# Kernel optimization log

Hardware: AMD Instinct MI355X
Metric: run time of the kernel (lower is better)

Reference implementation:

```python
import jax, jax.numpy as jnp
import numpy as np

N, E, D, H, HD, DFF = 2048, 32768, 256, 8, 32, 1024
NEG = -1e30  # masked-out logit (exp -> 0 in fp32)


def _layer_norm(x, w, b, eps=1e-5):
    mu = jnp.mean(x, axis=-1, keepdims=True)
    var = jnp.mean((x - mu) ** 2, axis=-1, keepdims=True)
    return (x - mu) * jax.lax.rsqrt(var + eps) * w + b


def setup_inputs() -> dict:
    key = jax.random.key(0)
    ks = jax.random.split(key, 24)
    w = lambda k, shape: (jax.random.normal(k, shape, dtype=jnp.float32) * 0.02)
    inp = {
        "node_feat": jax.random.normal(ks[0], (N, D), dtype=jnp.float32),
        "edge_feat": jax.random.normal(ks[1], (E, 10), dtype=jnp.float32),
        "src": jax.random.randint(ks[2], (E,), 0, N),
        "dst": jax.random.randint(ks[3], (E,), 0, N),
        "Wq": w(ks[4], (D, D)), "bq": jnp.zeros((D,), jnp.float32),
        "Wk": w(ks[5], (D, D)), "bk": jnp.zeros((D,), jnp.float32),
        "Wv": w(ks[6], (D, D)), "bv": jnp.zeros((D,), jnp.float32),
        "Wo": w(ks[7], (D, D)), "bo": jnp.zeros((D,), jnp.float32),
        "We": w(ks[8], (10, H)), "be": jnp.zeros((H,), jnp.float32),
        "n1w": jnp.ones((D,), jnp.float32), "n1b": jnp.zeros((D,), jnp.float32),
        "W1": w(ks[9], (D, DFF)), "b1": jnp.zeros((DFF,), jnp.float32),
        "W2": w(ks[10], (DFF, D)), "b2": jnp.zeros((D,), jnp.float32),
        "n2w": jnp.ones((D,), jnp.float32), "n2b": jnp.zeros((D,), jnp.float32),
    }
    return inp


def reference(node_feat, edge_feat, src, dst, Wq, bq, Wk, bk, Wv, bv, Wo, bo,
              We, be, n1w, n1b, W1, b1, W2, b2, n2w, n2b):
    n = node_feat.shape[0]
    Q = (node_feat @ Wq + bq).reshape(n, H, HD)
    K = (node_feat @ Wk + bk).reshape(n, H, HD)
    V = (node_feat @ Wv + bv).reshape(n, H, HD)

    # dense [n, n, H] scores (faithful to the original dense blowup)
    scores = jnp.einsum('ihd,jhd->ijh', Q, K) / np.sqrt(HD).astype(np.float32)

    # scatter edge bias into dense matrix (last-write semantics like torch indexing)
    edge_bias = edge_feat @ We + be                       # [E, H]
    bias = jnp.zeros((n, n, H), jnp.float32).at[src, dst].set(edge_bias)
    scores = scores + bias

    # symmetric adjacency mask with self-loops
    adj = jnp.zeros((n, n), jnp.float32)
    adj = adj.at[src, dst].set(1.0).at[dst, src].set(1.0)
    idx = jnp.arange(n)
    adj = adj.at[idx, idx].set(1.0)

    scores = jnp.where(adj[:, :, None] > 0, scores, NEG)
    attn = jax.nn.softmax(scores, axis=1)                 # softmax over j (dim=1)

    out = jnp.einsum('ijh,jhd->ihd', attn, V).reshape(n, D)
    out = out @ Wo + bo
    out = _layer_norm(out + node_feat, n1w, n1b)
    ffn = jax.nn.relu(out @ W1 + b1) @ W2 + b2
    out = _layer_norm(out + ffn, n2w, n2b)
    return out
```

## Files before the change

### kernel.cpp

```cpp
#include <hip/hip_runtime.h>
#include <hip/hip_bf16.h>

#define NN 2048
#define E_CNT 32768
#define D 256
#define DFF 1024
#define MAXN 256

typedef __hip_bfloat16 bf16;
typedef __attribute__((ext_vector_type(8))) short short8;
typedef __attribute__((ext_vector_type(4))) float f32x4;

__device__ __forceinline__ short bf2s(bf16 x) { union { bf16 b; short s; } u; u.b = x; return u.s; }
__device__ __forceinline__ float bs2f(unsigned short v) { return __uint_as_float(((unsigned)v) << 16); }

__device__ __forceinline__ int sniff_flag(const unsigned short* p, int* sh)
{
    int tid = threadIdx.x;
    int cnt = 0;
    for (int t = tid; t < 512; t += 256) {
        float f = bs2f(p[t]);
        if (!(fabsf(f) < 1000.f)) cnt++;
    }
#pragma unroll
    for (int off = 32; off > 0; off >>= 1) cnt += __shfl_down(cnt, off, 64);
    if ((tid & 63) == 0) sh[tid >> 6] = cnt;
    __syncthreads();
    int tot = sh[0] + sh[1] + sh[2] + sh[3];
    return tot > 16;
}

struct PrepArgs {
    const void* node; const void* edge;
    const int* src; const int* dst;
    const void* We; const void* be;
    const void* wsrc[6];
    const void* ssrc[10]; int sn[10]; int soff[10];
    bf16* node_b16; float* node_f32; float* smalls;
    short* wt; float* eb; int* pair; unsigned* bits;
    int* flagp;
};

__global__ __launch_bounds__(256) void k_prep(PrepArgs A)
{
    __shared__ int sh[4];
    __shared__ short tile[32][33];
    __shared__ float wsm[80], bbs[8];
    const int b = blockIdx.x;
    const int t = threadIdx.x;

    if (b >= 1408 && b < 1536) {
        int e = (b - 1408) * 256 + t;
        if (e < E_CNT) {
            int s = A.src[e], d = A.dst[e];
            atomicMax(&A.pair[(size_t)s * NN + d], e);
            atomicOr(&A.bits[s * 64 + (d >> 5)], 1u << (d & 31));
            atomicOr(&A.bits[d * 64 + (s >> 5)], 1u << (s & 31));
        }
        int n = (b - 1408) * 16 + (t >> 4);
        if (t < 128 && n < NN) atomicOr(&A.bits[n * 64 + (n >> 5)], 1u << (n & 31));
        return;
    }

    const int flag = sniff_flag((const unsigned short*)A.node, sh);

    if (b < 768) {
        int a, ti, ntn;
        if (b < 256)      { a = b >> 6; ti = b & 63;  ntn = 8;  }
        else if (b < 512) { a = 4;      ti = b - 256; ntn = 32; }
        else              { a = 5;      ti = b - 512; ntn = 8;  }
        const int Kd = (a == 5) ? 1024 : 256;
        const int Nd = (a == 4) ? 1024 : 256;
        int n0 = (ti % ntn) * 32, k0 = (ti / ntn) * 32;
        const void* s = A.wsrc[a];
        int c = t & 31, r4 = t >> 5;
#pragma unroll
        for (int p = 0; p < 4; p++) {
            int r = r4 + p * 8;
            short v;
            if (flag) v = bf2s(__float2bfloat16(((const float*)s)[(size_t)(k0 + r) * Nd + n0 + c]));
            else      v = ((const short*)s)[(size_t)(k0 + r) * Nd + n0 + c];
            tile[r][c] = v;
        }
        __syncthreads();
        static const int woff[6] = {0, 65536, 131072, 196608, 262144, 524288};
        short* dT = A.wt + woff[a];
#pragma unroll
        for (int p = 0; p < 4; p++) {
            int r = r4 + p * 8;
            dT[(size_t)(n0 + r) * Kd + k0 + c] = tile[c][r];
        }
        return;
    }
    if (b < 1024) {
        int i0 = (b - 768) * 2048 + t;
        if (flag) {
            const float* s = (const float*)A.node;
#pragma unroll
            for (int k = 0; k < 8; k++) A.node_b16[i0 + k * 256] = __float2bfloat16(s[i0 + k * 256]);
        } else {
            const short* s = (const short*)A.node;
            short* d = (short*)A.node_b16;
#pragma unroll
            for (int k = 0; k < 8; k++) d[i0 + k * 256] = s[i0 + k * 256];
        }
        return;
    }
    if (b < 1280) {
        int i0 = (b - 1024) * 2048 + t;
        if (flag) {
            const float* s = (const float*)A.node;
#pragma unroll
            for (int k = 0; k < 8; k++) A.node_f32[i0 + k * 256] = s[i0 + k * 256];
        } else {
            const bf16* s = (const bf16*)A.node;
#pragma unroll
            for (int k = 0; k < 8; k++) A.node_f32[i0 + k * 256] = __bfloat162float(s[i0 + k * 256]);
        }
        return;
    }
    if (b < 1408) {
        if (t < 80) wsm[t] = flag ? ((const float*)A.We)[t] : __bfloat162float(((const bf16*)A.We)[t]);
        if (t < 8)  bbs[t] = flag ? ((const float*)A.be)[t] : __bfloat162float(((const bf16*)A.be)[t]);
        __syncthreads();
        int e = (b - 1280) * 256 + t;
        float v[10];
        if (flag) {
            const float* ef = (const float*)A.edge;
#pragma unroll
            for (int k = 0; k < 10; k++) v[k] = ef[e * 10 + k];
        } else {
            const bf16* ef = (const bf16*)A.edge;
#pragma unroll
            for (int k = 0; k < 10; k++) v[k] = __bfloat162float(ef[e * 10 + k]);
        }
#pragma unroll
        for (int h = 0; h < 8; h++) {
            float s = bbs[h];
#pragma unroll
            for (int k = 0; k < 10; k++) s += v[k] * wsm[k * 8 + h];
            A.eb[e * 8 + h] = s;
        }
        return;
    }
    if (t == 0) *A.flagp = flag;
    for (int a = 0; a < 10; a++) {
        int n = A.sn[a];
        float* d = A.smalls + A.soff[a];
        if (flag) {
            const float* s = (const float*)A.ssrc[a];
            for (int i = t; i < n; i += 256) d[i] = s[i];
        } else {
            const bf16* s = (const bf16*)A.ssrc[a];
            for (int i = t; i < n; i += 256) d[i] = __bfloat162float(s[i]);
        }
    }
}

__global__ __launch_bounds__(256) void k_qkv3(
    const bf16* __restrict__ A,
    const bf16* __restrict__ WqT, const bf16* __restrict__ WkT, const bf16* __restrict__ WvT,
    const float* __restrict__ bq, const float* __restrict__ bk, const float* __restrict__ bv,
    bf16* __restrict__ Qb, bf16* __restrict__ Kb, bf16* __restrict__ Vb)
{
    int z = blockIdx.z;
    const bf16* BT = (z == 0) ? WqT : (z == 1) ? WkT : WvT;
    const float* bias = (z == 0) ? bq : (z == 1) ? bk : bv;
    bf16* C = (z == 0) ? Qb : (z == 1) ? Kb : Vb;
    __shared__ __align__(16) short As[2][4 * 64 * 8];
    __shared__ __align__(16) short Bs[2][4 * 32 * 8];
    int t = threadIdx.x, w = t >> 6, l = t & 63, fr = l & 15, fc = l >> 4;
    int i0 = blockIdx.x * 64, j0 = blockIdx.y * 32;
    int lr = t >> 2, lc = t & 3;
    f32x4 acc0 = {0.f, 0.f, 0.f, 0.f}, acc1 = {0.f, 0.f, 0.f, 0.f};
    const short* ap = (const short*)A + (size_t)(i0 + lr) * D + lc * 8;
    const short* bp = (const short*)BT + (size_t)(j0 + (lr & 31)) * D + lc * 8;
    for (int k0 = 0; k0 < D; k0 += 64) {
        short8 av0 = *(const short8*)(ap + k0);
        short8 av1 = *(const short8*)(ap + k0 + 32);
        short8 bv0 = {}, bv1 = {};
        if (t < 128) {
            bv0 = *(const short8*)(bp + k0);
            bv1 = *(const short8*)(bp + k0 + 32);
        }
        __syncthreads();
        *(short8*)&As[0][(lc * 64 + lr) * 8] = av0;
        *(short8*)&As[1][(lc * 64 + lr) * 8] = av1;
        if (t < 128) {
            *(short8*)&Bs[0][(lc * 32 + lr) * 8] = bv0;
            *(short8*)&Bs[1][(lc * 32 + lr) * 8] = bv1;
        }
        __syncthreads();
#pragma unroll
        for (int s = 0; s < 2; s++) {
            short8 af  = *(const short8*)&As[s][(fc * 64 + w * 16 + fr) * 8];
            short8 bf0 = *(const short8*)&Bs[s][(fc * 32 + fr) * 8];
            short8 bf1 = *(const short8*)&Bs[s][(fc * 32 + 16 + fr) * 8];
            acc0 = __builtin_amdgcn_mfma_f32_16x16x32_bf16(af, bf0, acc0, 0, 0, 0);
            acc1 = __builtin_amdgcn_mfma_f32_16x16x32_bf16(af, bf1, acc1, 0, 0, 0);
        }
    }
    float bb0 = bias[j0 + fr], bb1 = bias[j0 + 16 + fr];
    int orow = i0 + w * 16 + fc * 4;
#pragma unroll
    for (int j = 0; j < 4; j++) {
        C[(size_t)(orow + j) * D + j0 + fr]      = __float2bfloat16(acc0[j] + bb0);
        C[(size_t)(orow + j) * D + j0 + 16 + fr] = __float2bfloat16(acc1[j] + bb1);
    }
}

template<int EPI>
__global__ __launch_bounds__(256) void k_gemm(
    const bf16* __restrict__ A, const bf16* __restrict__ BT,
    const float* __restrict__ bias, void* __restrict__ Cp, int N, int K)
{
    __shared__ __align__(16) short As[2][4 * 64 * 8];
    __shared__ __align__(16) short Bs[2][4 * 32 * 8];
    int t = threadIdx.x;
    int w = t >> 6, l = t & 63;
    int fr = l & 15, fc = l >> 4;
    int i0 = blockIdx.x * 64, j0 = blockIdx.y * 32;
    int lr = t >> 2, lc = t & 3;
    f32x4 acc0 = {0.f, 0.f, 0.f, 0.f}, acc1 = {0.f, 0.f, 0.f, 0.f};
    const short* ap = (const short*)A + (size_t)(i0 + lr) * K + lc * 8;
    const short* bp = (const short*)BT + (size_t)(j0 + (lr & 31)) * K + lc * 8;
    for (int k0 = 0; k0 < K; k0 += 64) {
        short8 av0 = *(const short8*)(ap + k0);
        short8 av1 = *(const short8*)(ap + k0 + 32);
        short8 bv0 = {}, bv1 = {};
        if (t < 128) {
            bv0 = *(const short8*)(bp + k0);
            bv1 = *(const short8*)(bp + k0 + 32);
        }
        __syncthreads();
        *(short8*)&As[0][(lc * 64 + lr) * 8] = av0;
        *(short8*)&As[1][(lc * 64 + lr) * 8] = av1;
        if (t < 128) {
            *(short8*)&Bs[0][(lc * 32 + lr) * 8] = bv0;
            *(short8*)&Bs[1][(lc * 32 + lr) * 8] = bv1;
        }
        __syncthreads();
#pragma unroll
        for (int s = 0; s < 2; s++) {
            short8 af  = *(const short8*)&As[s][(fc * 64 + w * 16 + fr) * 8];
            short8 bf0 = *(const short8*)&Bs[s][(fc * 32 + fr) * 8];
            short8 bf1 = *(const short8*)&Bs[s][(fc * 32 + 16 + fr) * 8];
            acc0 = __builtin_amdgcn_mfma_f32_16x16x32_bf16(af, bf0, acc0, 0, 0, 0);
            acc1 = __builtin_amdgcn_mfma_f32_16x16x32_bf16(af, bf1, acc1, 0, 0, 0);
        }
    }
    float bb0 = bias[j0 + fr];
    float bb1 = bias[j0 + 16 + fr];
    int orow = i0 + w * 16 + fc * 4;
    bf16* C = (bf16*)Cp;
#pragma unroll
    for (int j = 0; j < 4; j++) {
        C[(size_t)(orow + j) * N + j0 + fr]      = __float2bfloat16(fmaxf(acc0[j] + bb0, 0.f));
        C[(size_t)(orow + j) * N + j0 + 16 + fr] = __float2bfloat16(fmaxf(acc1[j] + bb1, 0.f));
    }
}

__global__ __launch_bounds__(256) void k_attn(
    const bf16* __restrict__ Q, const bf16* __restrict__ K,
    const bf16* __restrict__ V, const float* __restrict__ eb,
    const int* __restrict__ pair, const unsigned* __restrict__ bits,
    bf16* __restrict__ attn_out)
{
    int i = blockIdx.x;
    int tid = threadIdx.x;
    __shared__ float q[D];
    __shared__ int   nbr[MAXN];
    __shared__ int   eid[MAXN];
    __shared__ float sc[MAXN][8];
    __shared__ float lhi[8];
    __shared__ int   nn_s;
    q[tid] = bs2f(((const unsigned short*)Q)[(size_t)i * D + tid]);
    if (tid < 64) {
        unsigned wrd = bits[i * 64 + tid];
        int cnt = __popc(wrd);
        int pre = cnt;
#pragma unroll
        for (int off = 1; off < 64; off <<= 1) {
            int v = __shfl_up(pre, off, 64);
            if (tid >= off) pre += v;
        }
        int pos = pre - cnt;
        while (wrd) {
            int b = __ffs(wrd) - 1;
            wrd &= wrd - 1;
            if (pos < MAXN) nbr[pos] = tid * 32 + b;
            pos++;
        }
        if (tid == 63) nn_s = (pre < MAXN) ? pre : MAXN;
    }
    __syncthreads();
    int nn = nn_s;
    const size_t prow = (size_t)i * NN;
    for (int n = tid; n < nn; n += 256) eid[n] = pair[prow + nbr[n]];
    __syncthreads();
    const short* Ks = (const short*)K;
    for (int t2 = tid; t2 < nn * 8; t2 += 256) {
        int n = t2 >> 3, h = t2 & 7;
        int j = nbr[n];
        const short8* kr = (const short8*)(Ks + (size_t)j * D + h * 32);
        const float4* qr = (const float4*)(q + h * 32);
        float s = 0.f;
#pragma unroll
        for (int c = 0; c < 4; c++) {
            short8 kv = kr[c];
            float4 q0 = qr[c * 2], q1 = qr[c * 2 + 1];
            s += q0.x * bs2f((unsigned short)kv[0]) + q0.y * bs2f((unsigned short)kv[1])
               + q0.z * bs2f((unsigned short)kv[2]) + q0.w * bs2f((unsigned short)kv[3])
               + q1.x * bs2f((unsigned short)kv[4]) + q1.y * bs2f((unsigned short)kv[5])
               + q1.z * bs2f((unsigned short)kv[6]) + q1.w * bs2f((unsigned short)kv[7]);
        }
        s *= 0.17677669529663687f;
        int e = eid[n];
        if (e >= 0) s += eb[e * 8 + h];
        sc[n][h] = s;
    }
    __syncthreads();
    {
        int h = tid >> 5, l32 = tid & 31;
        float m = -1e30f;
        for (int n = l32; n < nn; n += 32) m = fmaxf(m, sc[n][h]);
#pragma unroll
        for (int off = 1; off < 32; off <<= 1) m = fmaxf(m, __shfl_xor(m, off, 64));
        float lsum = 0.f;
        for (int n = l32; n < nn; n += 32) {
            float e = __expf(sc[n][h] - m);
            sc[n][h] = e;
            lsum += e;
        }
#pragma unroll
        for (int off = 1; off < 32; off <<= 1) lsum += __shfl_xor(lsum, off, 64);
        if (l32 == 0) lhi[h] = 1.f / lsum;
    }
    __syncthreads();
    int h = tid >> 5;
    const unsigned short* Vu = (const unsigned short*)V;
    float acc = 0.f;
    int n = 0;
    for (; n + 4 <= nn; n += 4) {
        int j0 = nbr[n], j1 = nbr[n + 1], j2 = nbr[n + 2], j3 = nbr[n + 3];
        float p0 = sc[n][h], p1 = sc[n + 1][h], p2 = sc[n + 2][h], p3 = sc[n + 3][h];
        acc += p0 * bs2f(Vu[(size_t)j0 * D + tid]) + p1 * bs2f(Vu[(size_t)j1 * D + tid])
             + p2 * bs2f(Vu[(size_t)j2 * D + tid]) + p3 * bs2f(Vu[(size_t)j3 * D + tid]);
    }
    for (; n < nn; n++) acc += sc[n][h] * bs2f(Vu[(size_t)nbr[n] * D + tid]);
    attn_out[(size_t)i * D + tid] = __float2bfloat16(acc * lhi[h]);
}

template<int MODE, int KDIM>
__global__ __launch_bounds__(256) void k_gemmln(
    const bf16* __restrict__ A, const bf16* __restrict__ BT,
    const float* __restrict__ bias, const float* __restrict__ res,
    const float* __restrict__ lnw, const float* __restrict__ lnb,
    float* __restrict__ outf, bf16* __restrict__ outb, const int* __restrict__ flagp)
{
    __shared__ __align__(16) short As[4 * 32 * 8];
    __shared__ __align__(16) short Bs[4 * 256 * 8];
    __shared__ float Cs[32][257];
    int t = threadIdx.x;
    int w = t >> 6, l = t & 63, fr = l & 15, fc = l >> 4;
    int i0 = blockIdx.x * 32;
    int ar = t >> 2, akc = t & 3;
    f32x4 acc[2][4];
#pragma unroll
    for (int rt = 0; rt < 2; rt++)
#pragma unroll
        for (int c = 0; c < 4; c++) acc[rt][c] = {0.f, 0.f, 0.f, 0.f};
    const short* ap = (const short*)A + (size_t)(i0 + (ar & 31)) * KDIM + akc * 8;
    const short* bp = (const short*)BT;
    short8 av = {};
    if (t < 128) av = *(const short8*)(ap);
    short8 bv[4];
#pragma unroll
    for (int p = 0; p < 4; p++)
        bv[p] = *(const short8*)(bp + (size_t)(p * 64 + ar) * KDIM + akc * 8);
    for (int k0 = 0; k0 < KDIM; k0 += 32) {
        __syncthreads();
        if (t < 128) *(short8*)&As[(akc * 32 + ar) * 8] = av;
#pragma unroll
        for (int p = 0; p < 4; p++)
            *(short8*)&Bs[(akc * 256 + p * 64 + ar) * 8] = bv[p];
        __syncthreads();
        if (k0 + 32 < KDIM) {
            if (t < 128) av = *(const short8*)(ap + k0 + 32);
#pragma unroll
            for (int p = 0; p < 4; p++)
                bv[p] = *(const short8*)(bp + (size_t)(p * 64 + ar) * KDIM + k0 + 32 + akc * 8);
        }
        short8 af0 = *(const short8*)&As[(fc * 32 + fr) * 8];
        short8 af1 = *(const short8*)&As[(fc * 32 + 16 + fr) * 8];
#pragma unroll
        for (int c = 0; c < 4; c++) {
            int ct = w * 4 + c;
            short8 bfr = *(const short8*)&Bs[(fc * 256 + ct * 16 + fr) * 8];
            acc[0][c] = __builtin_amdgcn_mfma_f32_16x16x32_bf16(af0, bfr, acc[0][c], 0, 0, 0);
            acc[1][c] = __builtin_amdgcn_mfma_f32_16x16x32_bf16(af1, bfr, acc[1][c], 0, 0, 0);
        }
    }
#pragma unroll
    for (int rt = 0; rt < 2; rt++)
#pragma unroll
        for (int c = 0; c < 4; c++) {
            int ct = w * 4 + c;
            float bb = bias[ct * 16 + fr];
#pragma unroll
            for (int j = 0; j < 4; j++)
                Cs[rt * 16 + fc * 4 + j][ct * 16 + fr] = acc[rt][c][j] + bb;
        }
    __syncthreads();
    int r = t >> 3, c0 = t & 7;
    float vbuf[32];
    float s = 0.f, qq = 0.f;
#pragma unroll
    for (int m = 0; m < 32; m++) {
        int c = c0 + m * 8;
        float v = Cs[r][c] + res[(size_t)(i0 + r) * D + c];
        vbuf[m] = v;
        s += v; qq += v * v;
    }
#pragma unroll
    for (int off = 1; off < 8; off <<= 1) {
        s  += __shfl_xor(s, off, 64);
        qq += __shfl_xor(qq, off, 64);
    }
    float mu  = s * (1.f / D);
    float var = qq * (1.f / D) - mu * mu;
    float rsd = rsqrtf(var + 1e-5f);
    int flag = (MODE == 1) ? *flagp : 0;
#pragma unroll
    for (int m = 0; m < 32; m++) {
        int c = c0 + m * 8;
        float o = (vbuf[m] - mu) * rsd * lnw[c] + lnb[c];
        size_t idx = (size_t)(i0 + r) * D + c;
        if (MODE == 0) {
            outf[idx] = o;
            outb[idx] = __float2bfloat16(o);
        } else {
            if (flag) outf[idx] = o;
            else      outb[idx] = __float2bfloat16(o);
        }
    }
}

extern "C" void kernel_launch(void* const* d_in, const int* in_sizes, int n_in,
                              void* d_out, int out_size, void* d_ws, size_t ws_size,
                              hipStream_t stream)
{
    (void)in_sizes; (void)n_in; (void)out_size; (void)ws_size;

    char* ws = (char*)d_ws;
    const size_t KB = 1024;
    float*    conv     = (float*)ws;
    bf16*     node_b16 = (bf16*)(ws + 3584 * KB);
    short*    wt       = (short*)(ws + 4608 * KB);
    int*      flagp    = (int*)(ws + 6144 * KB);
    unsigned* bits     = (unsigned*)(ws + 6272 * KB);
    float*    eb       = (float*)(ws + 7168 * KB);
    bf16*     Qb       = (bf16*)(ws + 8192 * KB);
    bf16*     Kb       = (bf16*)(ws + 10240 * KB);
    bf16*     Vb       = (bf16*)(ws + 11264 * KB);
    bf16*     attn_out = (bf16*)(ws + 12288 * KB);
    float*    x1f      = (float*)(ws + 13312 * KB);
    bf16*     x1b      = (bf16*)(ws + 15360 * KB);
    int*      pair     = (int*)(ws + 16384 * KB);
    bf16*     hid      = (bf16*)(ws + 34816 * KB);

    float* node_f32 = conv;
    float* smalls   = conv + 524288;
    static const int sidx[10] = {5, 7, 9, 11, 14, 15, 17, 19, 20, 21};
    static const int ssz[10]  = {256, 256, 256, 256, 256, 256, 1024, 256, 256, 256};
    int soff[10]; int so = 0;
    for (int a = 0; a < 10; a++) { soff[a] = so; so += ssz[a]; }
    const float* fbq  = smalls + soff[0];
    const float* fbk  = smalls + soff[1];
    const float* fbv  = smalls + soff[2];
    const float* fbo  = smalls + soff[3];
    const float* fn1w = smalls + soff[4];
    const float* fn1b = smalls + soff[5];
    const float* fb1  = smalls + soff[6];
    const float* fb2  = smalls + soff[7];
    const float* fn2w = smalls + soff[8];
    const float* fn2b = smalls + soff[9];

    static const int widx[6] = {4, 6, 8, 10, 16, 18};
    const bf16* WqT = (const bf16*)(wt + 0);
    const bf16* WkT = (const bf16*)(wt + 65536);
    const bf16* WvT = (const bf16*)(wt + 131072);
    const bf16* WoT = (const bf16*)(wt + 196608);
    const bf16* W1T = (const bf16*)(wt + 262144);
    const bf16* W2T = (const bf16*)(wt + 524288);

    PrepArgs pa;
    pa.node = d_in[0]; pa.edge = d_in[1];
    pa.src = (const int*)d_in[2]; pa.dst = (const int*)d_in[3];
    pa.We = d_in[12]; pa.be = d_in[13];
    for (int a = 0; a < 6; a++)  pa.wsrc[a] = d_in[widx[a]];
    for (int a = 0; a < 10; a++) { pa.ssrc[a] = d_in[sidx[a]]; pa.sn[a] = ssz[a]; pa.soff[a] = soff[a]; }
    pa.node_b16 = node_b16; pa.node_f32 = node_f32; pa.smalls = smalls;
    pa.wt = wt; pa.eb = eb; pa.pair = pair; pa.bits = bits; pa.flagp = flagp;

    hipMemsetAsync(bits, 0x00, (size_t)NN * 64 * 4, stream);
    hipMemsetAsync(pair, 0xFF, (size_t)NN * NN * 4, stream);

    k_prep<<<1537, 256, 0, stream>>>(pa);
    k_qkv3<<<dim3(32, 8, 3), 256, 0, stream>>>(node_b16, WqT, WkT, WvT, fbq, fbk, fbv, Qb, Kb, Vb);
    k_attn<<<NN, 256, 0, stream>>>(Qb, Kb, Vb, eb, pair, bits, attn_out);
    k_gemmln<0, 256><<<64, 256, 0, stream>>>(attn_out, WoT, fbo, node_f32, fn1w, fn1b,
                                             x1f, x1b, flagp);
    k_gemm<1><<<dim3(32, 32), 256, 0, stream>>>(x1b, W1T, fb1, hid, DFF, D);
    k_gemmln<1, 1024><<<64, 256, 0, stream>>>(hid, W2T, fb2, x1f, fn2w, fn2b,
                                              (float*)d_out, (bf16*)d_out, flagp);
}
```

Measured before the change: 171.1 us.

## Split fused GEMM+LayerNorm into generic tiled GEMM and separate LayerNorm kernels

Replaces the fused GEMM+LayerNorm kernel, which launched only 64 blocks of 32 full-width rows, with the generic tiled GEMM kernel (256 blocks) writing fp32 results to workspace, followed by a lightweight wave-per-row LayerNorm kernel. The aim is more parallelism and better occupancy across the GPU for the Wo and W2 projections. The cost is two extra kernel launches and an fp32 round trip of the intermediate through global memory.

```diff
diff --git a/kernel.cpp b/kernel.cpp
--- a/kernel.cpp
+++ b/kernel.cpp
@@ -252,11 +252,20 @@
     float bb0 = bias[j0 + fr];
     float bb1 = bias[j0 + 16 + fr];
     int orow = i0 + w * 16 + fc * 4;
-    bf16* C = (bf16*)Cp;
-#pragma unroll
-    for (int j = 0; j < 4; j++) {
-        C[(size_t)(orow + j) * N + j0 + fr]      = __float2bfloat16(fmaxf(acc0[j] + bb0, 0.f));
-        C[(size_t)(orow + j) * N + j0 + 16 + fr] = __float2bfloat16(fmaxf(acc1[j] + bb1, 0.f));
+    if (EPI == 0) {
+        float* C = (float*)Cp;
+#pragma unroll
+        for (int j = 0; j < 4; j++) {
+            C[(size_t)(orow + j) * N + j0 + fr]      = acc0[j] + bb0;
+            C[(size_t)(orow + j) * N + j0 + 16 + fr] = acc1[j] + bb1;
+        }
+    } else {
+        bf16* C = (bf16*)Cp;
+#pragma unroll
+        for (int j = 0; j < 4; j++) {
+            C[(size_t)(orow + j) * N + j0 + fr]      = __float2bfloat16(fmaxf(acc0[j] + bb0, 0.f));
+            C[(size_t)(orow + j) * N + j0 + 16 + fr] = __float2bfloat16(fmaxf(acc1[j] + bb1, 0.f));
+        }
     }
 }
 
@@ -351,97 +360,50 @@
     attn_out[(size_t)i * D + tid] = __float2bfloat16(acc * lhi[h]);
 }
 
-template<int MODE, int KDIM>
-__global__ __launch_bounds__(256) void k_gemmln(
-    const bf16* __restrict__ A, const bf16* __restrict__ BT,
-    const float* __restrict__ bias, const float* __restrict__ res,
-    const float* __restrict__ lnw, const float* __restrict__ lnb,
-    float* __restrict__ outf, bf16* __restrict__ outb, const int* __restrict__ flagp)
-{
-    __shared__ __align__(16) short As[4 * 32 * 8];
-    __shared__ __align__(16) short Bs[4 * 256 * 8];
-    __shared__ float Cs[32][257];
-    int t = threadIdx.x;
-    int w = t >> 6, l = t & 63, fr = l & 15, fc = l >> 4;
-    int i0 = blockIdx.x * 32;
-    int ar = t >> 2, akc = t & 3;
-    f32x4 acc[2][4];
-#pragma unroll
-    for (int rt = 0; rt < 2; rt++)
-#pragma unroll
-        for (int c = 0; c < 4; c++) acc[rt][c] = {0.f, 0.f, 0.f, 0.f};
-    const short* ap = (const short*)A + (size_t)(i0 + (ar & 31)) * KDIM + akc * 8;
-    const short* bp = (const short*)BT;
-    short8 av = {};
-    if (t < 128) av = *(const short8*)(ap);
-    short8 bv[4];
-#pragma unroll
-    for (int p = 0; p < 4; p++)
-        bv[p] = *(const short8*)(bp + (size_t)(p * 64 + ar) * KDIM + akc * 8);
-    for (int k0 = 0; k0 < KDIM; k0 += 32) {
-        __syncthreads();
-        if (t < 128) *(short8*)&As[(akc * 32 + ar) * 8] = av;
-#pragma unroll
-        for (int p = 0; p < 4; p++)
-            *(short8*)&Bs[(akc * 256 + p * 64 + ar) * 8] = bv[p];
-        __syncthreads();
-        if (k0 + 32 < KDIM) {
-            if (t < 128) av = *(const short8*)(ap + k0 + 32);
-#pragma unroll
-            for (int p = 0; p < 4; p++)
-                bv[p] = *(const short8*)(bp + (size_t)(p * 64 + ar) * KDIM + k0 + 32 + akc * 8);
-        }
-        short8 af0 = *(const short8*)&As[(fc * 32 + fr) * 8];
-        short8 af1 = *(const short8*)&As[(fc * 32 + 16 + fr) * 8];
-#pragma unroll
-        for (int c = 0; c < 4; c++) {
-            int ct = w * 4 + c;
-            short8 bfr = *(const short8*)&Bs[(fc * 256 + ct * 16 + fr) * 8];
-            acc[0][c] = __builtin_amdgcn_mfma_f32_16x16x32_bf16(af0, bfr, acc[0][c], 0, 0, 0);
-            acc[1][c] = __builtin_amdgcn_mfma_f32_16x16x32_bf16(af1, bfr, acc[1][c], 0, 0, 0);
-        }
-    }
-#pragma unroll
-    for (int rt = 0; rt < 2; rt++)
-#pragma unroll
-        for (int c = 0; c < 4; c++) {
-            int ct = w * 4 + c;
-            float bb = bias[ct * 16 + fr];
-#pragma unroll
-            for (int j = 0; j < 4; j++)
-                Cs[rt * 16 + fc * 4 + j][ct * 16 + fr] = acc[rt][c][j] + bb;
-        }
-    __syncthreads();
-    int r = t >> 3, c0 = t & 7;
-    float vbuf[32];
-    float s = 0.f, qq = 0.f;
-#pragma unroll
-    for (int m = 0; m < 32; m++) {
-        int c = c0 + m * 8;
-        float v = Cs[r][c] + res[(size_t)(i0 + r) * D + c];
-        vbuf[m] = v;
-        s += v; qq += v * v;
-    }
-#pragma unroll
-    for (int off = 1; off < 8; off <<= 1) {
-        s  += __shfl_xor(s, off, 64);
-        qq += __shfl_xor(qq, off, 64);
+template<int MODE>
+__global__ __launch_bounds__(256) void k_ln(
+    const float* __restrict__ g, const float* __restrict__ res,
+    const float* __restrict__ w, const float* __restrict__ b,
+    float* __restrict__ xf, bf16* __restrict__ xb, const int* __restrict__ flagp)
+{
+    int row = blockIdx.x * 4 + (threadIdx.x >> 6);
+    int l = threadIdx.x & 63;
+    size_t base = (size_t)row * D + l * 4;
+    float4 gv = *(const float4*)(g + base);
+    float4 rv = *(const float4*)(res + base);
+    float v0 = gv.x + rv.x, v1 = gv.y + rv.y, v2 = gv.z + rv.z, v3 = gv.w + rv.w;
+    float s = v0 + v1 + v2 + v3;
+    float q = v0 * v0 + v1 * v1 + v2 * v2 + v3 * v3;
+#pragma unroll
+    for (int off = 32; off > 0; off >>= 1) {
+        s += __shfl_xor(s, off, 64);
+        q += __shfl_xor(q, off, 64);
     }
     float mu  = s * (1.f / D);
-    float var = qq * (1.f / D) - mu * mu;
-    float rsd = rsqrtf(var + 1e-5f);
-    int flag = (MODE == 1) ? *flagp : 0;
-#pragma unroll
-    for (int m = 0; m < 32; m++) {
-        int c = c0 + m * 8;
-        float o = (vbuf[m] - mu) * rsd * lnw[c] + lnb[c];
-        size_t idx = (size_t)(i0 + r) * D + c;
-        if (MODE == 0) {
-            outf[idx] = o;
-            outb[idx] = __float2bfloat16(o);
+    float var = q * (1.f / D) - mu * mu;
+    float rs  = rsqrtf(var + 1e-5f);
+    float4 wv = *(const float4*)(w + l * 4);
+    float4 bv = *(const float4*)(b + l * 4);
+    float o0 = (v0 - mu) * rs * wv.x + bv.x;
+    float o1 = (v1 - mu) * rs * wv.y + bv.y;
+    float o2 = (v2 - mu) * rs * wv.z + bv.z;
+    float o3 = (v3 - mu) * rs * wv.w + bv.w;
+    if (MODE == 0) {
+        float4 o; o.x = o0; o.y = o1; o.z = o2; o.w = o3;
+        *(float4*)(xf + base) = o;
+        xb[base + 0] = __float2bfloat16(o0);
+        xb[base + 1] = __float2bfloat16(o1);
+        xb[base + 2] = __float2bfloat16(o2);
+        xb[base + 3] = __float2bfloat16(o3);
+    } else {
+        if (*flagp) {
+            float4 o; o.x = o0; o.y = o1; o.z = o2; o.w = o3;
+            *(float4*)(xf + base) = o;
         } else {
-            if (flag) outf[idx] = o;
-            else      outb[idx] = __float2bfloat16(o);
+            xb[base + 0] = __float2bfloat16(o0);
+            xb[base + 1] = __float2bfloat16(o1);
+            xb[base + 2] = __float2bfloat16(o2);
+            xb[base + 3] = __float2bfloat16(o3);
         }
     }
 }
@@ -467,7 +429,9 @@
     float*    x1f      = (float*)(ws + 13312 * KB);
     bf16*     x1b      = (bf16*)(ws + 15360 * KB);
     int*      pair     = (int*)(ws + 16384 * KB);
+    float*    g2       = (float*)(ws + 32768 * KB);
     bf16*     hid      = (bf16*)(ws + 34816 * KB);
+    float*    g4       = (float*)(ws + 38912 * KB);
 
     float* node_f32 = conv;
     float* smalls   = conv + 524288;
@@ -509,9 +473,10 @@
     k_prep<<<1537, 256, 0, stream>>>(pa);
     k_qkv3<<<dim3(32, 8, 3), 256, 0, stream>>>(node_b16, WqT, WkT, WvT, fbq, fbk, fbv, Qb, Kb, Vb);
     k_attn<<<NN, 256, 0, stream>>>(Qb, Kb, Vb, eb, pair, bits, attn_out);
-    k_gemmln<0, 256><<<64, 256, 0, stream>>>(attn_out, WoT, fbo, node_f32, fn1w, fn1b,
-                                             x1f, x1b, flagp);
+
+    k_gemm<0><<<dim3(32, 8), 256, 0, stream>>>(attn_out, WoT, fbo, g2, D, D);
+    k_ln<0><<<NN / 4, 256, 0, stream>>>(g2, node_f32, fn1w, fn1b, x1f, x1b, flagp);
     k_gemm<1><<<dim3(32, 32), 256, 0, stream>>>(x1b, W1T, fb1, hid, DFF, D);
-    k_gemmln<1, 1024><<<64, 256, 0, stream>>>(hid, W2T, fb2, x1f, fn2w, fn2b,
-                                              (float*)d_out, (bf16*)d_out, flagp);
-}
+    k_gemm<0><<<dim3(32, 8), 256, 0, stream>>>(hid, W2T, fb2, g4, D, DFF);
+    k_ln<1><<<NN / 4, 256, 0, stream>>>(g4, x1f, fn2w, fn2b, (float*)d_out, (bf16*)d_out, flagp);
+}
```

After: 154.4 us. 9.7% less time.
